# Kernel optimization log

Measured on AMD Instinct MI355X. Metric: run time of the kernel, lower is better.

The kernel has to match this reference:

```python
import jax, jax.numpy as jnp
import numpy as np

N, IN_DIM, OUT_DIM = 4096, 512, 512
H, D = 8, OUT_DIM // 8          # num_heads, head_dim
ALPHA = 0.2                     # leaky relu slope
NEG = -9e15
EPS = 1e-5


def setup_inputs() -> dict:
    key = jax.random.key(0)
    k1, k2, k3, k4 = jax.random.split(key, 4)
    x = jax.random.normal(k1, (N, IN_DIM), dtype=jnp.float32)
    adj = jax.random.randint(k2, (N, N), 0, 2, dtype=jnp.int32)
    # scale params like nn.Linear default init (~1/sqrt(fan_in)) to keep scores sane
    W = jax.random.normal(k3, (OUT_DIM, IN_DIM), dtype=jnp.float32) / np.sqrt(IN_DIM)
    a = jax.random.normal(k4, (2 * D,), dtype=jnp.float32) / np.sqrt(2 * D)
    gamma = jnp.ones((OUT_DIM,), dtype=jnp.float32)
    beta = jnp.zeros((OUT_DIM,), dtype=jnp.float32)
    return {"x": x, "adj": adj, "W": W, "a": a, "gamma": gamma, "beta": beta}


def reference(x, adj, W, a, gamma, beta):
    n = x.shape[0]
    Wh = (x @ W.T).reshape(n, H, D)                       # [N, H, D]
    a_src, a_dst = a[:D], a[D:]                           # shared across heads
    s_src = jnp.einsum('jhd,d->jh', Wh, a_src)            # [N, H] source term
    s_dst = jnp.einsum('ihd,d->ih', Wh, a_dst)            # [N, H] dest term
    # e[i, j, h] = leakyrelu(a_src . Wh[j,h] + a_dst . Wh[i,h]); row i = dst, col j = src
    e = jax.nn.leaky_relu(s_dst[:, None, :] + s_src[None, :, :], negative_slope=ALPHA)
    e = jnp.where((adj > 0)[:, :, None], e, NEG)          # mask non-edges
    attn = jax.nn.softmax(e, axis=1)                      # softmax over source nodes j
    h_prime = jnp.einsum('ijh,jhd->ihd', attn, Wh).reshape(n, H * D)  # [N, out_dim]
    # BatchNorm1d (training-mode batch statistics, biased variance)
    mean = jnp.mean(h_prime, axis=0)
    var = jnp.var(h_prime, axis=0)
    h_prime = gamma * (h_prime - mean) * jax.lax.rsqrt(var + EPS) + beta
    return jax.nn.relu(h_prime)
```

## Files before the change

### kernel.cpp

```cpp
#include <hip/hip_runtime.h>
#include <hip/hip_bf16.h>
#include <stdint.h>


typedef __attribute__((ext_vector_type(4))) float f32x4;
typedef __attribute__((ext_vector_type(8))) short s16x8;

#define LOG2E 1.4426950408889634f

#if __has_builtin(__builtin_amdgcn_sbfe)
#define MASKQ(w, q) ((uint32_t)__builtin_amdgcn_sbfe((int)(w), (q), 1))
#else
#define MASKQ(w, q) ((uint32_t)(((int32_t)((w) << (31 - (q)))) >> 31))
#endif

static __device__ __forceinline__ ushort f2bf(float f) {
  union { float f; uint32_t u; } v; v.f = f;
  uint32_t r = (v.u + 0x7FFFu + ((v.u >> 16) & 1u)) >> 16;
  return (ushort)r;
}

static __device__ __forceinline__ short bf16b(float f) {
  __hip_bfloat16 h = __float2bfloat16(f);
  union { __hip_bfloat16 h; short s; } c; c.h = h;
  return c.s;
}

static __device__ __forceinline__ float bf2f(ushort u) {
  union { uint32_t u; float f; } c; c.u = ((uint32_t)u) << 16;
  return c.f;
}

static __device__ __forceinline__ void gl_lds16(const ushort* g, ushort* l) {
  __builtin_amdgcn_global_load_lds(
      (const __attribute__((address_space(1))) unsigned int*)(g),
      (__attribute__((address_space(3))) unsigned int*)(l), 16, 0, 0);
}

__global__ __launch_bounds__(256) void k_convert(const float* __restrict__ x,
                                                 const float* __restrict__ W,
                                                 ushort* __restrict__ xb,
                                                 ushort* __restrict__ wb) {
  const int idx = (blockIdx.x * 256 + threadIdx.x) * 4;
  const int NX = 4096 * 512;
  if (idx < NX) {
    float4 v = *(const float4*)(x + idx);
    ushort4 o; o.x = f2bf(v.x); o.y = f2bf(v.y); o.z = f2bf(v.z); o.w = f2bf(v.w);
    *(ushort4*)(xb + idx) = o;
  } else {
    const int k = idx - NX;
    float4 v = *(const float4*)(W + k);
    ushort4 o; o.x = f2bf(v.x); o.y = f2bf(v.y); o.z = f2bf(v.z); o.w = f2bf(v.w);
    *(ushort4*)(wb + k) = o;
  }
}

__global__ __launch_bounds__(256) void k_pack(const int* __restrict__ adj,
                                              unsigned long long* __restrict__ maskw,
                                              float* __restrict__ stats) {
  const int t = threadIdx.x;
  if (blockIdx.x == 0) {
    stats[t] = 0.f; stats[t + 256] = 0.f; stats[t + 512] = 0.f; stats[t + 768] = 0.f;
  }
  const size_t base = (size_t)blockIdx.x * 8192;
  const int lane = t & 63;
#pragma unroll 4
  for (int it = 0; it < 32; ++it) {
    const size_t elem = base + it * 256 + t;
    unsigned long long b = __ballot(adj[elem] > 0);
    if (lane == 0) maskw[elem >> 6] = b;
  }
}

__global__ __launch_bounds__(256) void k_gemm(const ushort* __restrict__ xb,
                                              const ushort* __restrict__ wb,
                                              const float* __restrict__ a,
                                              ushort* __restrict__ WhT,
                                              float* __restrict__ EsT,
                                              float* __restrict__ es2T,
                                              float* __restrict__ nEdT,
                                              float* __restrict__ rT) {
  __shared__ ushort bt[64 * 512];
  float* tl = (float*)bt;
  const int lane = threadIdx.x & 63;
  const int wv = threadIdx.x >> 6;
  const int l15 = lane & 15, lg = lane >> 4;
  const int m0 = blockIdx.x * 64;
  const int h = blockIdx.y;
  const int n0 = h * 64;

#pragma unroll
  for (int it = 0; it < 16; ++it) {
    const int col = it * 4 + wv;
    const ushort* src = wb + (size_t)(n0 + col) * 512 + (lane ^ (col & 7)) * 8;
    gl_lds16(src, &bt[col * 512]);
  }
  __syncthreads();

  const ushort* ap = xb + (size_t)(m0 + wv * 16 + l15) * 512 + lg * 8;
  f32x4 acc[4] = {};
  for (int k0 = 0; k0 < 512; k0 += 32) {
    s16x8 av = *(const s16x8*)(ap + k0);
#pragma unroll
    for (int ct = 0; ct < 4; ++ct) {
      const int col = ct * 16 + l15;
      s16x8 b = *(const s16x8*)((const char*)bt + col * 1024 +
                                (((k0 + lg * 8) * 2) ^ ((col & 7) << 4)));
      acc[ct] = __builtin_amdgcn_mfma_f32_16x16x32_bf16(av, b, acc[ct], 0, 0, 0);
    }
  }
  float aS[4], aD[4];
#pragma unroll
  for (int ct = 0; ct < 4; ++ct) {
    aS[ct] = a[ct * 16 + l15];
    aD[ct] = a[64 + ct * 16 + l15];
  }
#pragma unroll
  for (int r = 0; r < 4; ++r) {
    float s1 = acc[0][r] * aS[0] + acc[1][r] * aS[1] + acc[2][r] * aS[2] + acc[3][r] * aS[3];
    float s2 = acc[0][r] * aD[0] + acc[1][r] * aD[1] + acc[2][r] * aD[2] + acc[3][r] * aD[3];
#pragma unroll
    for (int off = 1; off < 16; off <<= 1) {
      s1 += __shfl_xor(s1, off);
      s2 += __shfl_xor(s2, off);
    }
    if (l15 == 0) {
      const int row = m0 + wv * 16 + lg * 4 + r;
      const float aa = s1 * LOG2E;
      const float bb = s2 * LOG2E;
      EsT[h * 4096 + row]  = __builtin_amdgcn_exp2f(aa);
      es2T[h * 4096 + row] = __builtin_amdgcn_exp2f(0.2f * aa);
      nEdT[h * 4096 + row] = __builtin_amdgcn_exp2f(-bb);
      rT[h * 4096 + row]   = __builtin_amdgcn_exp2f(-0.8f * bb);
    }
  }
  __syncthreads();
#pragma unroll
  for (int ct = 0; ct < 4; ++ct)
#pragma unroll
    for (int r = 0; r < 4; ++r)
      tl[(ct * 16 + l15) * 65 + wv * 16 + lg * 4 + r] = acc[ct][r];
  __syncthreads();
  const int c = threadIdx.x >> 2, mb = (threadIdx.x & 3) * 16;
  s16x8 o0, o1;
#pragma unroll
  for (int k = 0; k < 8; ++k) o0[k] = bf16b(tl[c * 65 + mb + k]);
#pragma unroll
  for (int k = 0; k < 8; ++k) o1[k] = bf16b(tl[c * 65 + mb + 8 + k]);
  *(s16x8*)(WhT + (size_t)(n0 + c) * 4096 + m0 + mb) = o0;
  *(s16x8*)(WhT + (size_t)(n0 + c) * 4096 + m0 + mb + 8) = o1;
}

__global__ __launch_bounds__(512, 4) void k_attn(
    const uint32_t* __restrict__ mask32,
    const ushort* __restrict__ WhT,
    const float* __restrict__ EsT,
    const float* __restrict__ es2T,
    const float* __restrict__ rT,
    ushort* __restrict__ num,
    float* __restrict__ lbuf) {
  __shared__ ushort tile[2][4096];
  __shared__ uint32_t mask_s[256 * 33];
  __shared__ float Es_s[1024];
  __shared__ float es2_s[1024];

  const int t = threadIdx.x;
  const int lane = t & 63, wv = t >> 6;
  const int l15 = lane & 15, lg = lane >> 4;
  const int h = blockIdx.y;
  const int jh = blockIdx.x & 3;
  const int ih = blockIdx.x >> 2;
  const int i0b = ih * 256;
  const int j0 = jh * 1024;

  if (t < 256) {
    *(float4*)&Es_s[t * 4] = *(const float4*)(EsT + h * 4096 + j0 + t * 4);
  } else {
    const int u = t - 256;
    *(float4*)&es2_s[u * 4] = *(const float4*)(es2T + h * 4096 + j0 + u * 4);
  }
  {
    const int r = t >> 1, part = t & 1;
    const uint32_t* src = mask32 + (size_t)(i0b + r) * 128 + jh * 32 + part * 16;
    uint32_t* dst = &mask_s[r * 33 + part * 16];
#pragma unroll
    for (int k = 0; k < 4; ++k)
      *(int4*)(dst + k * 4) = *(const int4*)(src + k * 4);
  }
  const int cg = (wv << 3) + (lane >> 3);
  const int gg = (lane & 7) ^ (cg & 7);
  const ushort* sbase = WhT + (size_t)(h * 64 + cg) * 4096 + j0 + gg * 8;
  ushort* ldst0 = &tile[0][wv * 512];
  ushort* ldst1 = &tile[1][wv * 512];

  gl_lds16(sbase, ldst0);
  __syncthreads();

  const int rloc = wv * 32 + l15;
  const float r0c = rT[h * 4096 + i0b + rloc];
  const float r1c = rT[h * 4096 + i0b + rloc + 16];

  f32x4 acc[2][4] = {};
  f32x4 accd0 = {}, accd1 = {};
  s16x8 bones;
  {
    const short v = (l15 == 0) ? (short)0x3F80 : (short)0;
    bones[0] = v; bones[1] = v; bones[2] = v; bones[3] = v;
    bones[4] = v; bones[5] = v; bones[6] = v; bones[7] = v;
  }
  int cur = 0;

#pragma unroll 1
  for (int c = 0; c < 16; ++c) {
    if (c < 15) gl_lds16(sbase + (c + 1) * 64, cur ? ldst0 : ldst1);
#pragma unroll
    for (int half = 0; half < 2; ++half) {
      const int jsub = half * 32;
      const float4 eu = *(const float4*)&Es_s[c * 64 + jsub + lg * 8];
      const float4 ev = *(const float4*)&Es_s[c * 64 + jsub + lg * 8 + 4];
      const float4 fu = *(const float4*)&es2_s[c * 64 + jsub + lg * 8];
      const float4 fv = *(const float4*)&es2_s[c * 64 + jsub + lg * 8 + 4];
      const uint32_t w0 = mask_s[rloc * 33 + c * 2 + half] >> (lg * 8);
      const uint32_t w1 = mask_s[(rloc + 16) * 33 + c * 2 + half] >> (lg * 8);
      const char* tb = (const char*)&tile[cur][0];
      s16x8 b[4];
#pragma unroll
      for (int ct = 0; ct < 4; ++ct) {
        const int col = ct * 16 + l15;
        b[ct] = *(const s16x8*)(tb + col * 128 + ((jsub * 2 + lg * 16) ^ ((col & 7) << 4)));
      }
      const float E8[8] = {eu.x, eu.y, eu.z, eu.w, ev.x, ev.y, ev.z, ev.w};
      const float F8[8] = {fu.x, fu.y, fu.z, fu.w, fv.x, fv.y, fv.z, fv.w};
      union { s16x8 v8; uint32_t u32[4]; } pa0, pa1;
#pragma unroll
      for (int qp = 0; qp < 4; ++qp) {
        float z0[2], z1[2];
#pragma unroll
        for (int k = 0; k < 2; ++k) {
          const int q = qp * 2 + k;
          const float Eq = E8[q], Fq = F8[q];
          float t0 = fmaxf(Eq, r0c * Fq);
          z0[k] = __uint_as_float(MASKQ(w0, q) & __float_as_uint(t0));
          float t1 = fmaxf(Eq, r1c * Fq);
          z1[k] = __uint_as_float(MASKQ(w1, q) & __float_as_uint(t1));
        }
        union { __hip_bfloat162 h2; uint32_t u; } c0, c1;
        c0.h2 = __float22bfloat162_rn(make_float2(z0[0], z0[1]));
        c1.h2 = __float22bfloat162_rn(make_float2(z1[0], z1[1]));
        pa0.u32[qp] = c0.u;
        pa1.u32[qp] = c1.u;
      }
      accd0 = __builtin_amdgcn_mfma_f32_16x16x32_bf16(pa0.v8, bones, accd0, 0, 0, 0);
      accd1 = __builtin_amdgcn_mfma_f32_16x16x32_bf16(pa1.v8, bones, accd1, 0, 0, 0);
#pragma unroll
      for (int ct = 0; ct < 4; ++ct) {
        acc[0][ct] = __builtin_amdgcn_mfma_f32_16x16x32_bf16(pa0.v8, b[ct], acc[0][ct], 0, 0, 0);
        acc[1][ct] = __builtin_amdgcn_mfma_f32_16x16x32_bf16(pa1.v8, b[ct], acc[1][ct], 0, 0, 0);
      }
    }
    __syncthreads();
    cur ^= 1;
  }

  if (l15 == 0) {
    float* lb = &lbuf[((size_t)jh * 8 + h) * 4096 + i0b + rloc];
#pragma unroll
    for (int r = 0; r < 4; ++r) lb[lg * 4 + r] = accd0[r];
#pragma unroll
    for (int r = 0; r < 4; ++r) lb[16 + lg * 4 + r] = accd1[r];
  }
  ushort* np = num + (size_t)jh * 4096 * 512;
#pragma unroll
  for (int rs = 0; rs < 2; ++rs)
#pragma unroll
    for (int ct = 0; ct < 4; ++ct)
#pragma unroll
      for (int r = 0; r < 4; ++r)
        np[(size_t)(i0b + wv * 32 + rs * 16 + lg * 4 + r) * 512 + h * 64 + ct * 16 + l15] =
            (ushort)bf16b(acc[rs][ct][r]);
}

__global__ __launch_bounds__(512) void k_stats(const ushort* __restrict__ num,
                                               const float* __restrict__ lbuf,
                                               ushort* __restrict__ hpb,
                                               float* __restrict__ stats) {
  __shared__ float linv_s[128];
  const int t = threadIdx.x;
  const int r0 = blockIdx.x * 16;
  if (t < 128) {
    const int r = r0 + (t >> 3), hh = t & 7;
    float l = 0.f;
#pragma unroll
    for (int s = 0; s < 4; ++s) l += lbuf[((size_t)s * 8 + hh) * 4096 + r];
    linv_s[t] = 1.0f / l;
  }
  __syncthreads();
  const int c = t;
  const int hh = c >> 6;
  float s1 = 0.f, s2 = 0.f;
  for (int rr = 0; rr < 16; ++rr) {
    const int r = r0 + rr;
    float nsum = 0.f;
#pragma unroll
    for (int s = 0; s < 4; ++s)
      nsum += bf2f(num[(size_t)s * 4096 * 512 + (size_t)r * 512 + c]);
    const float v = nsum * linv_s[rr * 8 + hh];
    hpb[(size_t)r * 512 + c] = (ushort)bf16b(v);
    s1 += v; s2 += v * v;
  }
  atomicAdd(&stats[c], s1);
  atomicAdd(&stats[512 + c], s2);
}

__global__ __launch_bounds__(256) void k_apply(const ushort* __restrict__ hpb,
                                               const float* __restrict__ stats,
                                               const float* __restrict__ gamma,
                                               const float* __restrict__ beta,
                                               float* __restrict__ out) {
  const size_t idx8 = ((size_t)blockIdx.x * 256 + threadIdx.x) * 8;
  const int c0 = (int)(idx8 & 511);
  s16x8 hv = *(const s16x8*)(hpb + idx8);
#pragma unroll
  for (int k = 0; k < 8; ++k) {
    const int cc = c0 + k;
    const float mean = stats[cc] * (1.f / 4096.f);
    const float var = stats[512 + cc] * (1.f / 4096.f) - mean * mean;
    const float v = bf2f((ushort)hv[k]);
    const float val = (v - mean) * rsqrtf(var + 1e-5f) * gamma[cc] + beta[cc];
    out[idx8 + k] = fmaxf(val, 0.f);
  }
}

extern "C" void kernel_launch(void* const* d_in, const int* in_sizes, int n_in,
                              void* d_out, int out_size, void* d_ws, size_t ws_size,
                              hipStream_t stream) {
  const float* x = (const float*)d_in[0];
  const int* adj = (const int*)d_in[1];
  const float* W = (const float*)d_in[2];
  const float* a = (const float*)d_in[3];
  const float* gamma = (const float*)d_in[4];
  const float* beta = (const float*)d_in[5];
  float* out = (float*)d_out;

  char* ws = (char*)d_ws;
  size_t off = 0;
  auto alloc = [&](size_t bytes) -> void* {
    void* p = ws + off;
    off += (bytes + 255) & ~(size_t)255;
    return p;
  };
  ushort* WhT   = (ushort*)alloc((size_t)512 * 4096 * 2);
  float*  EsT   = (float*)alloc((size_t)8 * 4096 * 4);
  float*  es2T  = (float*)alloc((size_t)8 * 4096 * 4);
  float*  nEdT  = (float*)alloc((size_t)8 * 4096 * 4);
  float*  rT    = (float*)alloc((size_t)8 * 4096 * 4);
  unsigned long long* maskw = (unsigned long long*)alloc((size_t)4096 * 64 * 8);
  float*  lbuf  = (float*)alloc((size_t)32 * 4096 * 4);
  ushort* hpb   = (ushort*)alloc((size_t)4096 * 512 * 2);
  float*  stats = (float*)alloc((size_t)1024 * 4);
  const size_t ov = off;
  ushort* xb = (ushort*)(ws + ov);
  ushort* wb = (ushort*)(ws + ov + (size_t)4096 * 512 * 2);
  ushort* num = (ushort*)(ws + ov);

  hipLaunchKernelGGL(k_convert, dim3(2304), dim3(256), 0, stream, x, W, xb, wb);
  hipLaunchKernelGGL(k_pack, dim3(2048), dim3(256), 0, stream, adj, maskw, stats);
  hipLaunchKernelGGL(k_gemm, dim3(64, 8), dim3(256), 0, stream, xb, wb, a,
                     WhT, EsT, es2T, nEdT, rT);
  hipLaunchKernelGGL(k_attn, dim3(64, 8), dim3(512), 0, stream,
                     (const uint32_t*)maskw, WhT, EsT, es2T, rT, num, lbuf);
  hipLaunchKernelGGL(k_stats, dim3(256), dim3(512), 0, stream, num, lbuf, hpb, stats);
  hipLaunchKernelGGL(k_apply, dim3(1024), dim3(256), 0, stream, hpb, stats, gamma, beta, out);
}
```

Before: 85.10 us.

## Switch attention to fp16 packed math, deepen tile pipeline, fuse prep kernels

Result: faster. 75.20 us (-11.6%).

```diff
diff --git a/kernel.cpp b/kernel.cpp
--- a/kernel.cpp
+++ b/kernel.cpp
@@ -1,18 +1,14 @@
 #include <hip/hip_runtime.h>
 #include <hip/hip_bf16.h>
+#include <hip/hip_fp16.h>
 #include <stdint.h>
 
 
 typedef __attribute__((ext_vector_type(4))) float f32x4;
 typedef __attribute__((ext_vector_type(8))) short s16x8;
+typedef __attribute__((ext_vector_type(2))) _Float16 h2v;
 
 #define LOG2E 1.4426950408889634f
-
-#if __has_builtin(__builtin_amdgcn_sbfe)
-#define MASKQ(w, q) ((uint32_t)__builtin_amdgcn_sbfe((int)(w), (q), 1))
-#else
-#define MASKQ(w, q) ((uint32_t)(((int32_t)((w) << (31 - (q)))) >> 31))
-#endif
 
 static __device__ __forceinline__ ushort f2bf(float f) {
   union { float f; uint32_t u; } v; v.f = f;
@@ -31,44 +27,58 @@
   return c.f;
 }
 
+static __device__ __forceinline__ ushort hbits(float f) {
+  union { _Float16 h; ushort u; } c; c.h = (_Float16)f;
+  return c.u;
+}
+
+static __device__ __forceinline__ h2v u2h2(uint32_t u) {
+  union { uint32_t u; h2v h; } c; c.u = u; return c.h;
+}
+static __device__ __forceinline__ uint32_t h22u(h2v h) {
+  union { uint32_t u; h2v h; } c; c.h = h; return c.u;
+}
+
 static __device__ __forceinline__ void gl_lds16(const ushort* g, ushort* l) {
   __builtin_amdgcn_global_load_lds(
       (const __attribute__((address_space(1))) unsigned int*)(g),
       (__attribute__((address_space(3))) unsigned int*)(l), 16, 0, 0);
 }
 
-__global__ __launch_bounds__(256) void k_convert(const float* __restrict__ x,
-                                                 const float* __restrict__ W,
-                                                 ushort* __restrict__ xb,
-                                                 ushort* __restrict__ wb) {
-  const int idx = (blockIdx.x * 256 + threadIdx.x) * 4;
-  const int NX = 4096 * 512;
-  if (idx < NX) {
-    float4 v = *(const float4*)(x + idx);
-    ushort4 o; o.x = f2bf(v.x); o.y = f2bf(v.y); o.z = f2bf(v.z); o.w = f2bf(v.w);
-    *(ushort4*)(xb + idx) = o;
-  } else {
-    const int k = idx - NX;
-    float4 v = *(const float4*)(W + k);
-    ushort4 o; o.x = f2bf(v.x); o.y = f2bf(v.y); o.z = f2bf(v.z); o.w = f2bf(v.w);
-    *(ushort4*)(wb + k) = o;
-  }
-}
-
-__global__ __launch_bounds__(256) void k_pack(const int* __restrict__ adj,
+__global__ __launch_bounds__(256) void k_prep(const float* __restrict__ x,
+                                              const float* __restrict__ W,
+                                              const int* __restrict__ adj,
+                                              ushort* __restrict__ xb,
+                                              ushort* __restrict__ wb,
                                               unsigned long long* __restrict__ maskw,
                                               float* __restrict__ stats) {
   const int t = threadIdx.x;
-  if (blockIdx.x == 0) {
-    stats[t] = 0.f; stats[t + 256] = 0.f; stats[t + 512] = 0.f; stats[t + 768] = 0.f;
-  }
-  const size_t base = (size_t)blockIdx.x * 8192;
-  const int lane = t & 63;
+  if (blockIdx.x < 2304) {
+    const int idx = (blockIdx.x * 256 + t) * 4;
+    const int NX = 4096 * 512;
+    if (idx < NX) {
+      float4 v = *(const float4*)(x + idx);
+      ushort4 o; o.x = f2bf(v.x); o.y = f2bf(v.y); o.z = f2bf(v.z); o.w = f2bf(v.w);
+      *(ushort4*)(xb + idx) = o;
+    } else {
+      const int k = idx - NX;
+      float4 v = *(const float4*)(W + k);
+      ushort4 o; o.x = f2bf(v.x); o.y = f2bf(v.y); o.z = f2bf(v.z); o.w = f2bf(v.w);
+      *(ushort4*)(wb + k) = o;
+    }
+  } else {
+    const int pb = blockIdx.x - 2304;
+    if (pb == 0) {
+      stats[t] = 0.f; stats[t + 256] = 0.f; stats[t + 512] = 0.f; stats[t + 768] = 0.f;
+    }
+    const size_t base = (size_t)pb * 8192;
+    const int lane = t & 63;
 #pragma unroll 4
-  for (int it = 0; it < 32; ++it) {
-    const size_t elem = base + it * 256 + t;
-    unsigned long long b = __ballot(adj[elem] > 0);
-    if (lane == 0) maskw[elem >> 6] = b;
+    for (int it = 0; it < 32; ++it) {
+      const size_t elem = base + it * 256 + t;
+      unsigned long long b = __ballot(adj[elem] > 0);
+      if (lane == 0) maskw[elem >> 6] = b;
+    }
   }
 }
 
@@ -76,9 +86,8 @@
                                               const ushort* __restrict__ wb,
                                               const float* __restrict__ a,
                                               ushort* __restrict__ WhT,
-                                              float* __restrict__ EsT,
-                                              float* __restrict__ es2T,
-                                              float* __restrict__ nEdT,
+                                              ushort* __restrict__ EsT,
+                                              ushort* __restrict__ es2T,
                                               float* __restrict__ rT) {
   __shared__ ushort bt[64 * 512];
   float* tl = (float*)bt;
@@ -128,9 +137,8 @@
       const int row = m0 + wv * 16 + lg * 4 + r;
       const float aa = s1 * LOG2E;
       const float bb = s2 * LOG2E;
-      EsT[h * 4096 + row]  = __builtin_amdgcn_exp2f(aa);
-      es2T[h * 4096 + row] = __builtin_amdgcn_exp2f(0.2f * aa);
-      nEdT[h * 4096 + row] = __builtin_amdgcn_exp2f(-bb);
+      EsT[h * 4096 + row]  = hbits(__builtin_amdgcn_exp2f(aa));
+      es2T[h * 4096 + row] = hbits(__builtin_amdgcn_exp2f(0.2f * aa));
       rT[h * 4096 + row]   = __builtin_amdgcn_exp2f(-0.8f * bb);
     }
   }
@@ -144,9 +152,9 @@
   const int c = threadIdx.x >> 2, mb = (threadIdx.x & 3) * 16;
   s16x8 o0, o1;
 #pragma unroll
-  for (int k = 0; k < 8; ++k) o0[k] = bf16b(tl[c * 65 + mb + k]);
-#pragma unroll
-  for (int k = 0; k < 8; ++k) o1[k] = bf16b(tl[c * 65 + mb + 8 + k]);
+  for (int k = 0; k < 8; ++k) o0[k] = (short)hbits(tl[c * 65 + mb + k]);
+#pragma unroll
+  for (int k = 0; k < 8; ++k) o1[k] = (short)hbits(tl[c * 65 + mb + 8 + k]);
   *(s16x8*)(WhT + (size_t)(n0 + c) * 4096 + m0 + mb) = o0;
   *(s16x8*)(WhT + (size_t)(n0 + c) * 4096 + m0 + mb + 8) = o1;
 }
@@ -154,15 +162,15 @@
 __global__ __launch_bounds__(512, 4) void k_attn(
     const uint32_t* __restrict__ mask32,
     const ushort* __restrict__ WhT,
-    const float* __restrict__ EsT,
-    const float* __restrict__ es2T,
+    const ushort* __restrict__ EsT,
+    const ushort* __restrict__ es2T,
     const float* __restrict__ rT,
     ushort* __restrict__ num,
     float* __restrict__ lbuf) {
-  __shared__ ushort tile[2][4096];
+  __shared__ ushort tile[4][4096];
   __shared__ uint32_t mask_s[256 * 33];
-  __shared__ float Es_s[1024];
-  __shared__ float es2_s[1024];
+  __shared__ uint32_t Es_s[512];
+  __shared__ uint32_t es2_s[512];
 
   const int t = threadIdx.x;
   const int lane = t & 63, wv = t >> 6;
@@ -173,11 +181,10 @@
   const int i0b = ih * 256;
   const int j0 = jh * 1024;
 
-  if (t < 256) {
-    *(float4*)&Es_s[t * 4] = *(const float4*)(EsT + h * 4096 + j0 + t * 4);
-  } else {
-    const int u = t - 256;
-    *(float4*)&es2_s[u * 4] = *(const float4*)(es2T + h * 4096 + j0 + u * 4);
+  if (t < 128) {
+    ((uint4*)Es_s)[t] = ((const uint4*)EsT)[(h * 4096 + j0) / 8 + t];
+  } else if (t < 256) {
+    ((uint4*)es2_s)[t - 128] = ((const uint4*)es2T)[(h * 4096 + j0) / 8 + t - 128];
   }
   {
     const int r = t >> 1, part = t & 1;
@@ -190,76 +197,69 @@
   const int cg = (wv << 3) + (lane >> 3);
   const int gg = (lane & 7) ^ (cg & 7);
   const ushort* sbase = WhT + (size_t)(h * 64 + cg) * 4096 + j0 + gg * 8;
-  ushort* ldst0 = &tile[0][wv * 512];
-  ushort* ldst1 = &tile[1][wv * 512];
-
-  gl_lds16(sbase, ldst0);
+
+  gl_lds16(sbase, &tile[0][wv * 512]);
+  gl_lds16(sbase + 64, &tile[1][wv * 512]);
+  gl_lds16(sbase + 128, &tile[2][wv * 512]);
   __syncthreads();
 
   const int rloc = wv * 32 + l15;
-  const float r0c = rT[h * 4096 + i0b + rloc];
-  const float r1c = rT[h * 4096 + i0b + rloc + 16];
+  const float r0f = rT[h * 4096 + i0b + rloc];
+  const float r1f = rT[h * 4096 + i0b + rloc + 16];
+  const h2v r02 = {(_Float16)r0f, (_Float16)r0f};
+  const h2v r12 = {(_Float16)r1f, (_Float16)r1f};
 
   f32x4 acc[2][4] = {};
   f32x4 accd0 = {}, accd1 = {};
   s16x8 bones;
   {
-    const short v = (l15 == 0) ? (short)0x3F80 : (short)0;
+    const short v = (l15 == 0) ? (short)0x3C00 : (short)0;
     bones[0] = v; bones[1] = v; bones[2] = v; bones[3] = v;
     bones[4] = v; bones[5] = v; bones[6] = v; bones[7] = v;
   }
-  int cur = 0;
 
 #pragma unroll 1
   for (int c = 0; c < 16; ++c) {
-    if (c < 15) gl_lds16(sbase + (c + 1) * 64, cur ? ldst0 : ldst1);
+    if (c < 14)       asm volatile("s_waitcnt vmcnt(2)" ::: "memory");
+    else if (c == 14) asm volatile("s_waitcnt vmcnt(1)" ::: "memory");
+    else              asm volatile("s_waitcnt vmcnt(0)" ::: "memory");
+    __builtin_amdgcn_s_barrier();
+    if (c < 13) gl_lds16(sbase + (size_t)(c + 3) * 64, &tile[(c + 3) & 3][wv * 512]);
+    const char* tb = (const char*)&tile[c & 3][0];
 #pragma unroll
     for (int half = 0; half < 2; ++half) {
       const int jsub = half * 32;
-      const float4 eu = *(const float4*)&Es_s[c * 64 + jsub + lg * 8];
-      const float4 ev = *(const float4*)&Es_s[c * 64 + jsub + lg * 8 + 4];
-      const float4 fu = *(const float4*)&es2_s[c * 64 + jsub + lg * 8];
-      const float4 fv = *(const float4*)&es2_s[c * 64 + jsub + lg * 8 + 4];
+      const uint4 e4 = *(const uint4*)&Es_s[c * 32 + (jsub >> 1) + lg * 4];
+      const uint4 f4 = *(const uint4*)&es2_s[c * 32 + (jsub >> 1) + lg * 4];
       const uint32_t w0 = mask_s[rloc * 33 + c * 2 + half] >> (lg * 8);
       const uint32_t w1 = mask_s[(rloc + 16) * 33 + c * 2 + half] >> (lg * 8);
-      const char* tb = (const char*)&tile[cur][0];
       s16x8 b[4];
 #pragma unroll
       for (int ct = 0; ct < 4; ++ct) {
         const int col = ct * 16 + l15;
         b[ct] = *(const s16x8*)(tb + col * 128 + ((jsub * 2 + lg * 16) ^ ((col & 7) << 4)));
       }
-      const float E8[8] = {eu.x, eu.y, eu.z, eu.w, ev.x, ev.y, ev.z, ev.w};
-      const float F8[8] = {fu.x, fu.y, fu.z, fu.w, fv.x, fv.y, fv.z, fv.w};
       union { s16x8 v8; uint32_t u32[4]; } pa0, pa1;
 #pragma unroll
-      for (int qp = 0; qp < 4; ++qp) {
-        float z0[2], z1[2];
-#pragma unroll
-        for (int k = 0; k < 2; ++k) {
-          const int q = qp * 2 + k;
-          const float Eq = E8[q], Fq = F8[q];
-          float t0 = fmaxf(Eq, r0c * Fq);
-          z0[k] = __uint_as_float(MASKQ(w0, q) & __float_as_uint(t0));
-          float t1 = fmaxf(Eq, r1c * Fq);
-          z1[k] = __uint_as_float(MASKQ(w1, q) & __float_as_uint(t1));
-        }
-        union { __hip_bfloat162 h2; uint32_t u; } c0, c1;
-        c0.h2 = __float22bfloat162_rn(make_float2(z0[0], z0[1]));
-        c1.h2 = __float22bfloat162_rn(make_float2(z1[0], z1[1]));
-        pa0.u32[qp] = c0.u;
-        pa1.u32[qp] = c1.u;
+      for (int q2 = 0; q2 < 4; ++q2) {
+        const int q = q2 * 2;
+        const h2v e2 = u2h2(((const uint32_t*)&e4)[q2]);
+        const h2v f2 = u2h2(((const uint32_t*)&f4)[q2]);
+        const h2v t0 = __builtin_elementwise_max(e2, r02 * f2);
+        const h2v t1 = __builtin_elementwise_max(e2, r12 * f2);
+        const uint32_t mk0 = (((w0 >> q) & 1u) | (((w0 >> q) & 2u) << 15)) * 0xFFFFu;
+        const uint32_t mk1 = (((w1 >> q) & 1u) | (((w1 >> q) & 2u) << 15)) * 0xFFFFu;
+        pa0.u32[q2] = mk0 & h22u(t0);
+        pa1.u32[q2] = mk1 & h22u(t1);
       }
-      accd0 = __builtin_amdgcn_mfma_f32_16x16x32_bf16(pa0.v8, bones, accd0, 0, 0, 0);
-      accd1 = __builtin_amdgcn_mfma_f32_16x16x32_bf16(pa1.v8, bones, accd1, 0, 0, 0);
+      accd0 = __builtin_amdgcn_mfma_f32_16x16x32_f16(pa0.v8, bones, accd0, 0, 0, 0);
+      accd1 = __builtin_amdgcn_mfma_f32_16x16x32_f16(pa1.v8, bones, accd1, 0, 0, 0);
 #pragma unroll
       for (int ct = 0; ct < 4; ++ct) {
-        acc[0][ct] = __builtin_amdgcn_mfma_f32_16x16x32_bf16(pa0.v8, b[ct], acc[0][ct], 0, 0, 0);
-        acc[1][ct] = __builtin_amdgcn_mfma_f32_16x16x32_bf16(pa1.v8, b[ct], acc[1][ct], 0, 0, 0);
+        acc[0][ct] = __builtin_amdgcn_mfma_f32_16x16x32_f16(pa0.v8, b[ct], acc[0][ct], 0, 0, 0);
+        acc[1][ct] = __builtin_amdgcn_mfma_f32_16x16x32_f16(pa1.v8, b[ct], acc[1][ct], 0, 0, 0);
       }
     }
-    __syncthreads();
-    cur ^= 1;
   }
 
   if (l15 == 0) {
@@ -350,9 +350,8 @@
     return p;
   };
   ushort* WhT   = (ushort*)alloc((size_t)512 * 4096 * 2);
-  float*  EsT   = (float*)alloc((size_t)8 * 4096 * 4);
-  float*  es2T  = (float*)alloc((size_t)8 * 4096 * 4);
-  float*  nEdT  = (float*)alloc((size_t)8 * 4096 * 4);
+  ushort* EsT   = (ushort*)alloc((size_t)8 * 4096 * 2);
+  ushort* es2T  = (ushort*)alloc((size_t)8 * 4096 * 2);
   float*  rT    = (float*)alloc((size_t)8 * 4096 * 4);
   unsigned long long* maskw = (unsigned long long*)alloc((size_t)4096 * 64 * 8);
   float*  lbuf  = (float*)alloc((size_t)32 * 4096 * 4);
@@ -363,10 +362,10 @@
   ushort* wb = (ushort*)(ws + ov + (size_t)4096 * 512 * 2);
   ushort* num = (ushort*)(ws + ov);
 
-  hipLaunchKernelGGL(k_convert, dim3(2304), dim3(256), 0, stream, x, W, xb, wb);
-  hipLaunchKernelGGL(k_pack, dim3(2048), dim3(256), 0, stream, adj, maskw, stats);
+  hipLaunchKernelGGL(k_prep, dim3(4352), dim3(256), 0, stream,
+                     x, W, adj, xb, wb, maskw, stats);
   hipLaunchKernelGGL(k_gemm, dim3(64, 8), dim3(256), 0, stream, xb, wb, a,
-                     WhT, EsT, es2T, nEdT, rT);
+                     WhT, EsT, es2T, rT);
   hipLaunchKernelGGL(k_attn, dim3(64, 8), dim3(512), 0, stream,
                      (const uint32_t*)maskw, WhT, EsT, es2T, rT, num, lbuf);
   hipLaunchKernelGGL(k_stats, dim3(256), dim3(512), 0, stream, num, lbuf, hpb, stats);
```
